# Kernel tuning notes

Measured on AMD Instinct MI355X. Metric: run time of the kernel, lower is better.

The kernel has to match this reference:

```python
import jax, jax.numpy as jnp
import numpy as np

N, E, B, L = 32768, 524288, 64, 512  # nodes, edges, graphs, max nodes/graph
V, D, H = 10000, 256, 512            # vocab, embed_dim, hidden_dim


def gcn_conv(h, W, b, src, dst, n):
    """PyG GCNConv: add self-loops, symmetric deg normalization, scatter-sum."""
    h = h @ W  # [n, out]
    loops = jnp.arange(n)
    s = jnp.concatenate([src, loops])
    d = jnp.concatenate([dst, loops])
    deg = jax.ops.segment_sum(jnp.ones_like(d, dtype=h.dtype), d, num_segments=n)
    dinv = jnp.where(deg > 0, jax.lax.rsqrt(deg), 0.0)
    norm = dinv[s] * dinv[d]  # [E+n]
    out = jax.ops.segment_sum(h[s] * norm[:, None], d, num_segments=n)
    return out + b


def gru_seq(x, Wih, Whh, bih, bhh):
    """torch nn.GRU (1 layer, batch_first). x: [B, T, H] -> outputs [T, B, H]."""
    def step(h, x_t):
        gi = x_t @ Wih.T + bih          # [B, 3H]
        gh = h @ Whh.T + bhh            # [B, 3H]
        ir, iz, inn = jnp.split(gi, 3, axis=-1)
        hr, hz, hn = jnp.split(gh, 3, axis=-1)
        r = jax.nn.sigmoid(ir + hr)
        z = jax.nn.sigmoid(iz + hz)
        n = jnp.tanh(inn + r * hn)
        h = (1.0 - z) * n + z * h
        return h, h
    h0 = jnp.zeros((x.shape[0], Whh.shape[1]), x.dtype)
    _, outs = jax.lax.scan(step, h0, jnp.swapaxes(x, 0, 1))
    return outs  # [T, B, H]


def setup_inputs() -> dict:
    key = jax.random.key(0)
    ks = jax.random.split(key, 16)
    s = 0.05
    x = jax.random.randint(ks[0], (N,), 0, V)
    edge_index = jax.random.randint(ks[1], (2, E), 0, N)
    batch_idx = jnp.arange(N) // L  # sorted graph ids, L nodes per graph
    focal_points = jax.random.uniform(ks[2], (B, 1), jnp.float32)
    return {
        "x": x, "edge_index": edge_index, "batch_idx": batch_idx,
        "focal_points": focal_points,
        "emb": jax.random.normal(ks[3], (V, D), jnp.float32) * s,
        "W1": jax.random.normal(ks[4], (D, H), jnp.float32) * s,
        "b1": jnp.zeros((H,), jnp.float32),
        "W2": jax.random.normal(ks[5], (H, H), jnp.float32) * s,
        "b2": jnp.zeros((H,), jnp.float32),
        "Wih": jax.random.normal(ks[6], (3 * H, H), jnp.float32) * s,
        "Whh": jax.random.normal(ks[7], (3 * H, H), jnp.float32) * s,
        "bih": jnp.zeros((3 * H,), jnp.float32),
        "bhh": jnp.zeros((3 * H,), jnp.float32),
        "fc1_w": jax.random.normal(ks[8], (H + 1, H), jnp.float32) * s,
        "fc1_b": jnp.zeros((H,), jnp.float32),
        "fc2_w": jax.random.normal(ks[9], (H, 1), jnp.float32) * s,
        "fc2_b": jnp.zeros((1,), jnp.float32),
    }


def reference(x, edge_index, batch_idx, focal_points, emb, W1, b1, W2, b2,
              Wih, Whh, bih, bhh, fc1_w, fc1_b, fc2_w, fc2_b):
    src, dst = edge_index[0], edge_index[1]
    h = emb[x]  # [N, D]
    h = jax.nn.relu(gcn_conv(h, W1, b1, src, dst, N))
    h = jax.nn.relu(gcn_conv(h, W2, b2, src, dst, N))  # [N, H]

    # Ragged -> padded: scatter each node to (graph, position-within-graph)
    ones = jnp.ones((N,), h.dtype)
    counts = jax.ops.segment_sum(ones, batch_idx, num_segments=B)
    starts = jnp.cumsum(counts) - counts  # exclusive cumsum
    pos = jnp.arange(N) - starts[batch_idx].astype(jnp.int32)
    padded = jnp.zeros((B, L, H), h.dtype).at[batch_idx, pos].set(h)

    gru_out = gru_seq(padded, Wih, Whh, bih, bhh)   # [L, B, H]
    graph_emb = gru_out.mean(axis=0)                # [B, H]
    g = jnp.concatenate([graph_emb, focal_points], axis=1)  # [B, H+1]
    out = jax.nn.relu(g @ fc1_w + fc1_b)
    out = jax.nn.sigmoid(out @ fc2_w + fc2_b)       # [B, 1]
    return out
```

## Files before the change

### kernel.cpp

```cpp
#include <hip/hip_runtime.h>

#define NODES 32768
#define EDGES 524288
#define BGR   64
#define LSEQ  512
#define DEMB  256
#define HDIM  512

typedef unsigned short u16;
typedef unsigned int   u32;
typedef unsigned long long u64;
typedef __attribute__((ext_vector_type(8))) short short8;
typedef __attribute__((ext_vector_type(4))) float f32x4;

__device__ __forceinline__ float bf2f(u16 u){ u32 x = ((u32)u)<<16; float f; __builtin_memcpy(&f,&x,4); return f; }
__device__ __forceinline__ u16 f2bf(float f){ u32 x; __builtin_memcpy(&x,&f,4); u32 r = x + 0x7fffu + ((x>>16)&1u); return (u16)(r>>16); }
__device__ __forceinline__ float lo16(u32 u){ u32 x = u<<16; float f; __builtin_memcpy(&f,&x,4); return f; }
__device__ __forceinline__ float hi16(u32 u){ u32 x = u & 0xffff0000u; float f; __builtin_memcpy(&f,&x,4); return f; }
__device__ __forceinline__ u32 pack2(float a, float b){ return (u32)f2bf(a) | ((u32)f2bf(b)<<16); }


__global__ void zero_i32(int* p, int n){
  int i = blockIdx.x*256 + threadIdx.x;
  if (i < n) p[i] = 0;
}

__global__ void transpose_cast(const float* __restrict__ in, u16* __restrict__ out, int K, int N){
  int i = blockIdx.x*256 + threadIdx.x;
  if (i < N*K){ int n = i / K, k = i - n*K; out[i] = f2bf(in[(size_t)k*N + n]); }
}

__global__ void cast_bf(const float* __restrict__ in, u16* __restrict__ out, int n){
  int i = blockIdx.x*256 + threadIdx.x;
  if (i < n) out[i] = f2bf(in[i]);
}

__global__ void count_indeg(const int* __restrict__ dst, int* __restrict__ indeg){
  int e = blockIdx.x*256 + threadIdx.x;
  if (e < EDGES) atomicAdd(&indeg[dst[e]], 1);
}

__global__ void compute_dinv(const int* __restrict__ indeg, float* __restrict__ dinv){
  int i = blockIdx.x*256 + threadIdx.x;
  if (i < NODES) dinv[i] = rsqrtf((float)(indeg[i] + 1));
}

__global__ __launch_bounds__(1024) void scan_csr(const int* __restrict__ indeg,
                                                 int* __restrict__ row_ptr,
                                                 int* __restrict__ cursor){
  __shared__ int part[1024];
  int tid = threadIdx.x, base = tid*32;
  int loc[32]; int s = 0;
  for (int i=0;i<32;i++){ loc[i] = s; s += indeg[base+i]; }
  part[tid] = s; __syncthreads();
  for (int off=1; off<1024; off<<=1){
    int v = part[tid]; int add = (tid>=off) ? part[tid-off] : 0;
    __syncthreads(); part[tid] = v + add; __syncthreads();
  }
  int offt = (tid==0) ? 0 : part[tid-1];
  for (int i=0;i<32;i++){ int v = offt + loc[i]; row_ptr[base+i] = v; cursor[base+i] = v; }
}

__global__ void fill_csr(const int* __restrict__ src, const int* __restrict__ dst,
                         int* __restrict__ cursor, int* __restrict__ csr_src){
  int e = blockIdx.x*256 + threadIdx.x;
  if (e < EDGES){ int d = dst[e]; int p = atomicAdd(&cursor[d], 1); csr_src[p] = src[e]; }
}

__global__ __launch_bounds__(256) void agg_emb(const int* __restrict__ x, const u16* __restrict__ embb,
    const float* __restrict__ dinv, const int* __restrict__ row_ptr, const int* __restrict__ indeg,
    const int* __restrict__ csr_src, u16* __restrict__ out){
  int node = blockIdx.x*4 + (threadIdx.x>>6);
  int lane = threadIdx.x & 63;
  float di = dinv[node];
  int xi = x[node];
  u64 hv = *(const u64*)(embb + (size_t)xi*DEMB + lane*4);
  u32 h0 = (u32)hv, h1 = (u32)(hv>>32);
  float a0 = lo16(h0)*di, a1 = hi16(h0)*di, a2 = lo16(h1)*di, a3 = hi16(h1)*di;
  int st = row_ptr[node], cn = indeg[node];
  for (int p = st; p < st+cn; p++){
    int s = csr_src[p];
    float ws = dinv[s];
    u64 v = *(const u64*)(embb + (size_t)x[s]*DEMB + lane*4);
    u32 w0 = (u32)v, w1 = (u32)(v>>32);
    a0 += lo16(w0)*ws; a1 += hi16(w0)*ws; a2 += lo16(w1)*ws; a3 += hi16(w1)*ws;
  }
  u64 pv = (u64)pack2(a0*di,a1*di) | ((u64)pack2(a2*di,a3*di)<<32);
  *(u64*)(out + (size_t)node*DEMB + lane*4) = pv;
}

__global__ __launch_bounds__(256) void agg_h(const u16* __restrict__ hin, const float* __restrict__ dinv,
    const int* __restrict__ row_ptr, const int* __restrict__ indeg,
    const int* __restrict__ csr_src, u16* __restrict__ out){
  int node = blockIdx.x*4 + (threadIdx.x>>6);
  int lane = threadIdx.x & 63;
  float di = dinv[node];
  float a[8];
  uint4 hv = *((const uint4*)(hin + (size_t)node*HDIM) + lane);
  a[0]=lo16(hv.x)*di; a[1]=hi16(hv.x)*di; a[2]=lo16(hv.y)*di; a[3]=hi16(hv.y)*di;
  a[4]=lo16(hv.z)*di; a[5]=hi16(hv.z)*di; a[6]=lo16(hv.w)*di; a[7]=hi16(hv.w)*di;
  int st = row_ptr[node], cn = indeg[node];
  for (int p = st; p < st+cn; p++){
    int s = csr_src[p];
    float ws = dinv[s];
    uint4 v = *((const uint4*)(hin + (size_t)s*HDIM) + lane);
    a[0]+=lo16(v.x)*ws; a[1]+=hi16(v.x)*ws; a[2]+=lo16(v.y)*ws; a[3]+=hi16(v.y)*ws;
    a[4]+=lo16(v.z)*ws; a[5]+=hi16(v.z)*ws; a[6]+=lo16(v.w)*ws; a[7]+=hi16(v.w)*ws;
  }
  uint4 o; o.x=pack2(a[0]*di,a[1]*di); o.y=pack2(a[2]*di,a[3]*di);
  o.z=pack2(a[4]*di,a[5]*di); o.w=pack2(a[6]*di,a[7]*di);
  *(uint4*)(out + (size_t)node*HDIM + lane*8) = o;
}

#define BM 128
#define BN 128
#define BKK 32
__global__ __launch_bounds__(256) void gemm_bt(const u16* __restrict__ A, const u16* __restrict__ BT,
    const float* __restrict__ bias, u16* __restrict__ C, int M, int N, int K, int relu){
  __shared__ u16 aS[BM][BKK+8];
  __shared__ u16 bS[BN][BKK+8];
  int tid = threadIdx.x;
  int m0 = blockIdx.y * BM, n0 = blockIdx.x * BN;
  int lane = tid & 63, w = tid >> 6;
  int wm = w >> 1, wn = w & 1;
  f32x4 acc[4][4];
  for (int i=0;i<4;i++) for (int j=0;j<4;j++) acc[i][j] = (f32x4)0.0f;

  int r  = tid >> 1;
  int cc = (tid & 1) * 16;
  const u16* Ag = A + (size_t)(m0 + r) * K + cc;
  const u16* Bg = BT + (size_t)(n0 + r) * K + cc;
  int l15 = lane & 15, q8 = (lane >> 4) * 8;

  for (int k0 = 0; k0 < K; k0 += BKK) {
    uint4 av0 = *(const uint4*)(Ag + k0);
    uint4 av1 = *(const uint4*)(Ag + k0 + 8);
    uint4 bv0 = *(const uint4*)(Bg + k0);
    uint4 bv1 = *(const uint4*)(Bg + k0 + 8);
    *(uint4*)&aS[r][cc]   = av0; *(uint4*)&aS[r][cc+8] = av1;
    *(uint4*)&bS[r][cc]   = bv0; *(uint4*)&bS[r][cc+8] = bv1;
    __syncthreads();
    short8 af[4], bfr[4];
    for (int i=0;i<4;i++) af[i]  = *(const short8*)&aS[wm*64 + i*16 + l15][q8];
    for (int j=0;j<4;j++) bfr[j] = *(const short8*)&bS[wn*64 + j*16 + l15][q8];
    for (int i=0;i<4;i++)
      for (int j=0;j<4;j++)
        acc[i][j] = __builtin_amdgcn_mfma_f32_16x16x32_bf16(af[i], bfr[j], acc[i][j], 0, 0, 0);
    __syncthreads();
  }
  int q = lane >> 4;
  for (int i=0;i<4;i++) for (int j=0;j<4;j++){
    int col = n0 + wn*64 + j*16 + l15;
    float bval = bias[col];
    for (int rr=0; rr<4; rr++){
      int row = m0 + wm*64 + i*16 + q*4 + rr;
      float v = acc[i][j][rr] + bval;
      if (relu) v = fmaxf(v, 0.f);
      C[(size_t)row * N + col] = f2bf(v);
    }
  }
}

__global__ __launch_bounds__(512) void gru_kernel(const u16* __restrict__ gi,
    const float* __restrict__ Whh, const float* __restrict__ bhh,
    float* __restrict__ graph_emb, u64* __restrict__ xbuf){
  __shared__ u16  w_lds[96*520];
  __shared__ u16  h_lds[16*520];
  __shared__ float gh_lds[16*100];

  int tid = threadIdx.x;
  int g = blockIdx.x >> 4, j = blockIdx.x & 15;
  int lane = tid & 63, wave = tid >> 6;

  for (int idx = tid; idx < 96*512; idx += 512){
    int rr = idx >> 9, c = idx & 511;
    int grow = (rr >> 5) * 512 + j*32 + (rr & 31);
    w_lds[rr*520 + c] = f2bf(Whh[(size_t)grow*512 + c]);
  }
  for (int idx = tid; idx < 16*520; idx += 512) h_lds[idx] = 0;

  int b = tid >> 5, hh = tid & 31;
  int bg = g*16 + b;
  int c_r = j*32 + hh, c_z = 512 + j*32 + hh, c_n = 1024 + j*32 + hh;
  float bias_r = bhh[c_r], bias_z = bhh[c_z], bias_n = bhh[c_n];
  const u16* gi_row = gi + (size_t)bg * LSEQ * 1536;
  float h_prev = 0.f, accm = 0.f;
  int l15 = lane & 15, q8 = (lane>>4)*8, qr = (lane>>4)*4;

  u64* xb = xbuf + (size_t)g * 8192;
  u16 g_r = gi_row[c_r], g_z = gi_row[c_z], g_n = gi_row[c_n];

  __syncthreads();

  for (int t = 0; t < LSEQ; t++){
    if (wave < 6){
      f32x4 acc0 = (f32x4)0.0f, acc1 = (f32x4)0.0f;
      const u16* wrow = &w_lds[(wave*16 + l15)*520];
      const u16* hrow = &h_lds[l15*520];
      #pragma unroll
      for (int k0 = 0; k0 < 256; k0 += 32){
        acc0 = __builtin_amdgcn_mfma_f32_16x16x32_bf16(*(const short8*)(hrow + k0 + q8),
                                                       *(const short8*)(wrow + k0 + q8), acc0, 0, 0, 0);
        acc1 = __builtin_amdgcn_mfma_f32_16x16x32_bf16(*(const short8*)(hrow + 256 + k0 + q8),
                                                       *(const short8*)(wrow + 256 + k0 + q8), acc1, 0, 0, 0);
      }
      f32x4 acc = acc0 + acc1;
      int col = wave*16 + l15;
      #pragma unroll
      for (int rr2 = 0; rr2 < 4; rr2++) gh_lds[(qr + rr2)*100 + col] = acc[rr2];
    }
    __syncthreads();

    float ghr = gh_lds[b*100 + hh]      + bias_r;
    float ghz = gh_lds[b*100 + 32 + hh] + bias_z;
    float ghn = gh_lds[b*100 + 64 + hh] + bias_n;
    float rg = 1.f / (1.f + __expf(-(bf2f(g_r) + ghr)));
    float zg = 1.f / (1.f + __expf(-(bf2f(g_z) + ghz)));
    float pre = bf2f(g_n) + rg * ghn;
    pre = fminf(fmaxf(pre, -20.f), 20.f);
    float e2 = __expf(2.f * pre);
    float nn = (e2 - 1.f) / (e2 + 1.f);
    float h_new = (1.f - zg) * nn + zg * h_prev;
    accm += h_new; h_prev = h_new;

    u32 tag = (u32)(t + 1);
    float h_nb = __shfl_xor(h_new, 1, 64);
    if ((hh & 1) == 0){
      u64 val = ((u64)tag << 32) | (u64)pack2(h_new, h_nb);
      __hip_atomic_store(xb + (size_t)((t&1)*16 + b)*256 + j*16 + (hh>>1), val,
                         __ATOMIC_RELAXED, __HIP_MEMORY_SCOPE_AGENT);
    }

    int tn = (t + 1 < LSEQ) ? t + 1 : t;
    const u16* gp2 = gi_row + (size_t)tn * 1536;
    u16 n_r = gp2[c_r], n_z = gp2[c_z], n_n = gp2[c_n];

    const u64* rp = xb + (size_t)((t&1)*16 + b)*256 + hh*8;
    u64 v[8];
    bool ok;
    do {
      #pragma unroll
      for (int i=0;i<8;i++) v[i] = __hip_atomic_load(rp + i, __ATOMIC_RELAXED, __HIP_MEMORY_SCOPE_AGENT);
      ok = true;
      #pragma unroll
      for (int i=0;i<8;i++) ok = ok && ((u32)(v[i] >> 32) == tag);
    } while (!ok);

    u32* hl = (u32*)h_lds + b*260 + hh*8;
    #pragma unroll
    for (int i=0;i<8;i++) hl[i] = (u32)v[i];
    __syncthreads();

    g_r = n_r; g_z = n_z; g_n = n_n;
  }
  graph_emb[(size_t)bg*512 + j*32 + hh] = accm * (1.f/512.f);
}

__global__ __launch_bounds__(256) void head(const float* __restrict__ graph_emb, const float* __restrict__ focal,
    const float* __restrict__ fc1w, const float* __restrict__ fc1b,
    const float* __restrict__ fc2w, const float* __restrict__ fc2b, float* __restrict__ out){
  __shared__ float gv[513];
  __shared__ float h1s[512];
  __shared__ float red[4];
  int bq = blockIdx.x, tid = threadIdx.x;
  for (int i = tid; i < 512; i += 256) gv[i] = graph_emb[(size_t)bq*512 + i];
  if (tid == 0) gv[512] = focal[bq];
  __syncthreads();
  for (int c = tid; c < 512; c += 256){
    float acc = fc1b[c];
    for (int k = 0; k < 513; k++) acc += gv[k] * fc1w[(size_t)k*512 + c];
    h1s[c] = fmaxf(acc, 0.f);
  }
  __syncthreads();
  float p = h1s[tid]*fc2w[tid] + h1s[tid+256]*fc2w[tid+256];
  for (int off = 32; off; off >>= 1) p += __shfl_down(p, off, 64);
  if ((tid & 63) == 0) red[tid >> 6] = p;
  __syncthreads();
  if (tid == 0){
    float s = red[0]+red[1]+red[2]+red[3] + fc2b[0];
    out[bq] = 1.f / (1.f + __expf(-s));
  }
}

extern "C" void kernel_launch(void* const* d_in, const int* in_sizes, int n_in,
                              void* d_out, int out_size, void* d_ws, size_t ws_size,
                              hipStream_t stream){
  const int*   x     = (const int*)d_in[0];
  const int*   edge  = (const int*)d_in[1];
  const int*   srcp  = edge;
  const int*   dstp  = edge + EDGES;
  const float* focal = (const float*)d_in[3];
  const float* emb   = (const float*)d_in[4];
  const float* W1    = (const float*)d_in[5];
  const float* b1    = (const float*)d_in[6];
  const float* W2    = (const float*)d_in[7];
  const float* b2    = (const float*)d_in[8];
  const float* Wih   = (const float*)d_in[9];
  const float* Whh   = (const float*)d_in[10];
  const float* bih   = (const float*)d_in[11];
  const float* bhh   = (const float*)d_in[12];
  const float* fc1w  = (const float*)d_in[13];
  const float* fc1b  = (const float*)d_in[14];
  const float* fc2w  = (const float*)d_in[15];
  const float* fc2b  = (const float*)d_in[16];

  char* ws = (char*)d_ws;
  constexpr size_t H2_OFF    = 0;
  constexpr size_t AGG1_OFF  = 33554432;
  constexpr size_t H1_OFF    = 50331648;
  constexpr size_t AGG2_OFF  = 83886080;
  constexpr size_t GI_OFF    = 33554432;
  constexpr size_t MISC      = 134217728;
  constexpr size_t INDEG_OFF = MISC;
  constexpr size_t CNT_OFF   = MISC + 131072;
  constexpr size_t DINV_OFF  = MISC + 131328;
  constexpr size_t ROWPTR_OFF= MISC + 262400;
  constexpr size_t CURSOR_OFF= MISC + 393472;
  constexpr size_t CSR_OFF   = MISC + 524544;
  constexpr size_t W1T_OFF   = MISC + 2621696;
  constexpr size_t W2T_OFF   = MISC + 2883840;
  constexpr size_t WIHB_OFF  = MISC + 3408128;
  constexpr size_t XBUF_OFF  = MISC + 4980992;
  constexpr size_t GEMB_OFF  = MISC + 5243136;

  int*   indeg  = (int*)(ws + INDEG_OFF);
  float* dinv   = (float*)(ws + DINV_OFF);
  int*   rowptr = (int*)(ws + ROWPTR_OFF);
  int*   cursor = (int*)(ws + CURSOR_OFF);
  int*   csrsrc = (int*)(ws + CSR_OFF);
  u16*   W1T    = (u16*)(ws + W1T_OFF);
  u16*   W2T    = (u16*)(ws + W2T_OFF);
  u16*   WihB   = (u16*)(ws + WIHB_OFF);
  u16*   agg1   = (u16*)(ws + AGG1_OFF);
  u16*   h1     = (u16*)(ws + H1_OFF);
  u16*   agg2   = (u16*)(ws + AGG2_OFF);
  u16*   embb   = (u16*)(ws + AGG2_OFF);
  u16*   h2     = (u16*)(ws + H2_OFF);
  u16*   gi     = (u16*)(ws + GI_OFF);
  u64*   xbuf   = (u64*)(ws + XBUF_OFF);
  float* gemb   = (float*)(ws + GEMB_OFF);

  zero_i32<<<129, 256, 0, stream>>>(indeg, 32768 + 64);
  transpose_cast<<<512, 256, 0, stream>>>(W1, W1T, 256, 512);
  transpose_cast<<<1024, 256, 0, stream>>>(W2, W2T, 512, 512);
  cast_bf<<<3072, 256, 0, stream>>>(Wih, WihB, 1536*512);
  cast_bf<<<10000, 256, 0, stream>>>(emb, embb, 10000*256);
  count_indeg<<<2048, 256, 0, stream>>>(dstp, indeg);
  compute_dinv<<<128, 256, 0, stream>>>(indeg, dinv);
  scan_csr<<<1, 1024, 0, stream>>>(indeg, rowptr, cursor);
  fill_csr<<<2048, 256, 0, stream>>>(srcp, dstp, cursor, csrsrc);
  agg_emb<<<8192, 256, 0, stream>>>(x, embb, dinv, rowptr, indeg, csrsrc, agg1);
  gemm_bt<<<dim3(4, 256), 256, 0, stream>>>(agg1, W1T, b1, h1, NODES, 512, 256, 1);
  agg_h<<<8192, 256, 0, stream>>>(h1, dinv, rowptr, indeg, csrsrc, agg2);
  gemm_bt<<<dim3(4, 256), 256, 0, stream>>>(agg2, W2T, b2, h2, NODES, 512, 512, 1);
  gemm_bt<<<dim3(12, 256), 256, 0, stream>>>(h2, WihB, bih, gi, NODES, 1536, 512, 0);
  gru_kernel<<<64, 512, 0, stream>>>(gi, Whh, bhh, gemb, xbuf);
  head<<<64, 256, 0, stream>>>(gemb, focal, fc1w, fc1b, fc2w, fc2b, (float*)d_out);
}
```

Before: 2.587 ms.

## Pre-swizzle GRU weights and hidden state in LDS, double-buffer h, prefetch gi two steps ahead

Stores the recurrent weight slice and the hidden state in LDS in an MFMA-fragment-major layout, padded to 65 entries, so each lane does one contiguous 16-byte load per operand with fewer bank conflicts. The hidden state is double-buffered by timestep parity, and each lane writes its received values as two uint4 stores. The input-gate values are now prefetched two steps ahead instead of one to hide global load latency in the serial recurrence. An unused offset constant is removed. The cost is extra registers and a more complex indexing scheme.

```diff
diff --git a/kernel.cpp b/kernel.cpp
--- a/kernel.cpp
+++ b/kernel.cpp
@@ -164,20 +164,26 @@
 __global__ __launch_bounds__(512) void gru_kernel(const u16* __restrict__ gi,
     const float* __restrict__ Whh, const float* __restrict__ bhh,
     float* __restrict__ graph_emb, u64* __restrict__ xbuf){
-  __shared__ u16  w_lds[96*520];
-  __shared__ u16  h_lds[16*520];
+  __shared__ __align__(16) u16 w_swz[6*16*65*8];
+  __shared__ __align__(16) u16 h_swz[2][16*65*8];
   __shared__ float gh_lds[16*100];
 
   int tid = threadIdx.x;
   int g = blockIdx.x >> 4, j = blockIdx.x & 15;
   int lane = tid & 63, wave = tid >> 6;
-
-  for (int idx = tid; idx < 96*512; idx += 512){
-    int rr = idx >> 9, c = idx & 511;
-    int grow = (rr >> 5) * 512 + j*32 + (rr & 31);
-    w_lds[rr*520 + c] = f2bf(Whh[(size_t)grow*512 + c]);
-  }
-  for (int idx = tid; idx < 16*520; idx += 512) h_lds[idx] = 0;
+  int l15 = lane & 15, qr = (lane>>4)*4;
+
+  for (int s = tid; s < 6144; s += 512){
+    int w = s >> 10, rem = s & 1023, kc = rem >> 6, l = rem & 63;
+    int row = l & 15, qq = l >> 4;
+    int gate = w >> 1, half = w & 1;
+    int c = gate*512 + j*32 + half*16 + row;
+    const float* srcp = Whh + (size_t)c*512 + kc*32 + qq*8;
+    u16* dst = w_swz + ((size_t)(w*16 + kc)*65 + l)*8;
+    #pragma unroll
+    for (int i2 = 0; i2 < 8; i2++) dst[i2] = f2bf(srcp[i2]);
+  }
+  for (int i2 = tid; i2 < 16*65*8; i2 += 512) h_swz[0][i2] = 0;
 
   int b = tid >> 5, hh = tid & 31;
   int bg = g*16 + b;
@@ -185,24 +191,36 @@
   float bias_r = bhh[c_r], bias_z = bhh[c_z], bias_n = bhh[c_n];
   const u16* gi_row = gi + (size_t)bg * LSEQ * 1536;
   float h_prev = 0.f, accm = 0.f;
-  int l15 = lane & 15, q8 = (lane>>4)*8, qr = (lane>>4)*4;
 
   u64* xb = xbuf + (size_t)g * 8192;
-  u16 g_r = gi_row[c_r], g_z = gi_row[c_z], g_n = gi_row[c_n];
+
+  u16 gr0 = gi_row[c_r], gz0 = gi_row[c_z], gn0 = gi_row[c_n];
+  const u16* gp1 = gi_row + 1536;
+  u16 gr1 = gp1[c_r], gz1 = gp1[c_z], gn1 = gp1[c_n];
+
+  int kcc = hh >> 1, qa = (hh & 1) * 2;
+  int cb0 = (kcc*65 + (qa  )*16 + b) * 4;
+  int cb1 = (kcc*65 + (qa+1)*16 + b) * 4;
 
   __syncthreads();
 
   for (int t = 0; t < LSEQ; t++){
+    int tn = (t + 2 < LSEQ) ? t + 2 : t;
+    const u16* gp2 = gi_row + (size_t)tn * 1536;
+    u16 nr = gp2[c_r], nz = gp2[c_z], nn2 = gp2[c_n];
+
     if (wave < 6){
+      const u16* hb = h_swz[t & 1];
+      const u16* wb = w_swz + (size_t)wave*16*65*8;
       f32x4 acc0 = (f32x4)0.0f, acc1 = (f32x4)0.0f;
-      const u16* wrow = &w_lds[(wave*16 + l15)*520];
-      const u16* hrow = &h_lds[l15*520];
       #pragma unroll
-      for (int k0 = 0; k0 < 256; k0 += 32){
-        acc0 = __builtin_amdgcn_mfma_f32_16x16x32_bf16(*(const short8*)(hrow + k0 + q8),
-                                                       *(const short8*)(wrow + k0 + q8), acc0, 0, 0, 0);
-        acc1 = __builtin_amdgcn_mfma_f32_16x16x32_bf16(*(const short8*)(hrow + 256 + k0 + q8),
-                                                       *(const short8*)(wrow + 256 + k0 + q8), acc1, 0, 0, 0);
+      for (int kc = 0; kc < 8; kc++){
+        acc0 = __builtin_amdgcn_mfma_f32_16x16x32_bf16(
+                 *(const short8*)(hb + ((size_t)kc*65 + lane)*8),
+                 *(const short8*)(wb + ((size_t)kc*65 + lane)*8), acc0, 0, 0, 0);
+        acc1 = __builtin_amdgcn_mfma_f32_16x16x32_bf16(
+                 *(const short8*)(hb + ((size_t)(kc+8)*65 + lane)*8),
+                 *(const short8*)(wb + ((size_t)(kc+8)*65 + lane)*8), acc1, 0, 0, 0);
       }
       f32x4 acc = acc0 + acc1;
       int col = wave*16 + l15;
@@ -214,9 +232,9 @@
     float ghr = gh_lds[b*100 + hh]      + bias_r;
     float ghz = gh_lds[b*100 + 32 + hh] + bias_z;
     float ghn = gh_lds[b*100 + 64 + hh] + bias_n;
-    float rg = 1.f / (1.f + __expf(-(bf2f(g_r) + ghr)));
-    float zg = 1.f / (1.f + __expf(-(bf2f(g_z) + ghz)));
-    float pre = bf2f(g_n) + rg * ghn;
+    float rg = 1.f / (1.f + __expf(-(bf2f(gr0) + ghr)));
+    float zg = 1.f / (1.f + __expf(-(bf2f(gz0) + ghz)));
+    float pre = bf2f(gn0) + rg * ghn;
     pre = fminf(fmaxf(pre, -20.f), 20.f);
     float e2 = __expf(2.f * pre);
     float nn = (e2 - 1.f) / (e2 + 1.f);
@@ -230,10 +248,6 @@
       __hip_atomic_store(xb + (size_t)((t&1)*16 + b)*256 + j*16 + (hh>>1), val,
                          __ATOMIC_RELAXED, __HIP_MEMORY_SCOPE_AGENT);
     }
-
-    int tn = (t + 1 < LSEQ) ? t + 1 : t;
-    const u16* gp2 = gi_row + (size_t)tn * 1536;
-    u16 n_r = gp2[c_r], n_z = gp2[c_z], n_n = gp2[c_n];
 
     const u64* rp = xb + (size_t)((t&1)*16 + b)*256 + hh*8;
     u64 v[8];
@@ -246,12 +260,15 @@
       for (int i=0;i<8;i++) ok = ok && ((u32)(v[i] >> 32) == tag);
     } while (!ok);
 
-    u32* hl = (u32*)h_lds + b*260 + hh*8;
-    #pragma unroll
-    for (int i=0;i<8;i++) hl[i] = (u32)v[i];
+    u32* hl = (u32*)h_swz[(t+1) & 1];
+    uint4 w0; w0.x = (u32)v[0]; w0.y = (u32)v[1]; w0.z = (u32)v[2]; w0.w = (u32)v[3];
+    uint4 w1; w1.x = (u32)v[4]; w1.y = (u32)v[5]; w1.z = (u32)v[6]; w1.w = (u32)v[7];
+    *(uint4*)(hl + cb0) = w0;
+    *(uint4*)(hl + cb1) = w1;
     __syncthreads();
 
-    g_r = n_r; g_z = n_z; g_n = n_n;
+    gr0 = gr1; gz0 = gz1; gn0 = gn1;
+    gr1 = nr;  gz1 = nz;  gn1 = nn2;
   }
   graph_emb[(size_t)bg*512 + j*32 + hh] = accm * (1.f/512.f);
 }
@@ -312,7 +329,6 @@
   constexpr size_t GI_OFF    = 33554432;
   constexpr size_t MISC      = 134217728;
   constexpr size_t INDEG_OFF = MISC;
-  constexpr size_t CNT_OFF   = MISC + 131072;
   constexpr size_t DINV_OFF  = MISC + 131328;
   constexpr size_t ROWPTR_OFF= MISC + 262400;
   constexpr size_t CURSOR_OFF= MISC + 393472;
```

After: 2.729 ms. 1.05x slower.

## Split GRU recurrence across twice as many blocks with K-split MFMA waves

Applied to the files above, without the earlier changes.

The persistent GRU kernel now uses 32 blocks per group of 16 graphs instead of 16, so each block owns 16 hidden columns rather than 32. The six waves now split the K dimension in half per gate, writing two partial gh buffers that are summed in the gate computation. This shortens each block's per-step serial matvec chain and spreads the work over more CUs. In exchange, the cross-block flag exchange each step involves more participants, and half the threads sit idle during the gate math. It also vectorizes the LDS writes of the exchanged hidden state.

```diff
diff --git a/kernel.cpp b/kernel.cpp
--- a/kernel.cpp
+++ b/kernel.cpp
@@ -164,78 +164,84 @@
 __global__ __launch_bounds__(512) void gru_kernel(const u16* __restrict__ gi,
     const float* __restrict__ Whh, const float* __restrict__ bhh,
     float* __restrict__ graph_emb, u64* __restrict__ xbuf){
-  __shared__ u16  w_lds[96*520];
+  __shared__ u16  w_lds[48*520];
   __shared__ u16  h_lds[16*520];
-  __shared__ float gh_lds[16*100];
+  __shared__ float gh_lds[2][16*52];
 
   int tid = threadIdx.x;
-  int g = blockIdx.x >> 4, j = blockIdx.x & 15;
+  int g = blockIdx.x >> 5, j = blockIdx.x & 31;
   int lane = tid & 63, wave = tid >> 6;
-
-  for (int idx = tid; idx < 96*512; idx += 512){
+  int l15 = lane & 15, q8 = (lane>>4)*8, qr = (lane>>4)*4;
+
+  for (int idx = tid; idx < 48*512; idx += 512){
     int rr = idx >> 9, c = idx & 511;
-    int grow = (rr >> 5) * 512 + j*32 + (rr & 31);
+    int grow = (rr >> 4) * 512 + j*16 + (rr & 15);
     w_lds[rr*520 + c] = f2bf(Whh[(size_t)grow*512 + c]);
   }
   for (int idx = tid; idx < 16*520; idx += 512) h_lds[idx] = 0;
 
-  int b = tid >> 5, hh = tid & 31;
-  int bg = g*16 + b;
-  int c_r = j*32 + hh, c_z = 512 + j*32 + hh, c_n = 1024 + j*32 + hh;
-  float bias_r = bhh[c_r], bias_z = bhh[c_z], bias_n = bhh[c_n];
+  int b = tid >> 4, hh = tid & 15;
+  int bg = g*16 + (b & 15);
+  int c_r = j*16 + hh, c_z = 512 + j*16 + hh, c_n = 1024 + j*16 + hh;
+  float bias_r = 0.f, bias_z = 0.f, bias_n = 0.f;
+  if (tid < 256){ bias_r = bhh[c_r]; bias_z = bhh[c_z]; bias_n = bhh[c_n]; }
   const u16* gi_row = gi + (size_t)bg * LSEQ * 1536;
   float h_prev = 0.f, accm = 0.f;
-  int l15 = lane & 15, q8 = (lane>>4)*8, qr = (lane>>4)*4;
+
+  int pb = tid >> 5, ph = tid & 31;
 
   u64* xb = xbuf + (size_t)g * 8192;
-  u16 g_r = gi_row[c_r], g_z = gi_row[c_z], g_n = gi_row[c_n];
+
+  u16 gr0 = 0, gz0 = 0, gn0 = 0;
+  if (tid < 256){ gr0 = gi_row[c_r]; gz0 = gi_row[c_z]; gn0 = gi_row[c_n]; }
 
   __syncthreads();
 
   for (int t = 0; t < LSEQ; t++){
     if (wave < 6){
-      f32x4 acc0 = (f32x4)0.0f, acc1 = (f32x4)0.0f;
-      const u16* wrow = &w_lds[(wave*16 + l15)*520];
-      const u16* hrow = &h_lds[l15*520];
+      int gate = wave >> 1, kh = wave & 1;
+      const u16* wrow = &w_lds[(gate*16 + l15)*520 + kh*256];
+      const u16* hrow = &h_lds[l15*520 + kh*256];
+      f32x4 acc = (f32x4)0.0f;
       #pragma unroll
-      for (int k0 = 0; k0 < 256; k0 += 32){
-        acc0 = __builtin_amdgcn_mfma_f32_16x16x32_bf16(*(const short8*)(hrow + k0 + q8),
-                                                       *(const short8*)(wrow + k0 + q8), acc0, 0, 0, 0);
-        acc1 = __builtin_amdgcn_mfma_f32_16x16x32_bf16(*(const short8*)(hrow + 256 + k0 + q8),
-                                                       *(const short8*)(wrow + 256 + k0 + q8), acc1, 0, 0, 0);
-      }
-      f32x4 acc = acc0 + acc1;
-      int col = wave*16 + l15;
+      for (int kc = 0; kc < 8; kc++)
+        acc = __builtin_amdgcn_mfma_f32_16x16x32_bf16(*(const short8*)(hrow + kc*32 + q8),
+                                                      *(const short8*)(wrow + kc*32 + q8), acc, 0, 0, 0);
+      int col = gate*16 + l15;
       #pragma unroll
-      for (int rr2 = 0; rr2 < 4; rr2++) gh_lds[(qr + rr2)*100 + col] = acc[rr2];
+      for (int rr2 = 0; rr2 < 4; rr2++) gh_lds[kh][(qr + rr2)*52 + col] = acc[rr2];
     }
     __syncthreads();
 
-    float ghr = gh_lds[b*100 + hh]      + bias_r;
-    float ghz = gh_lds[b*100 + 32 + hh] + bias_z;
-    float ghn = gh_lds[b*100 + 64 + hh] + bias_n;
-    float rg = 1.f / (1.f + __expf(-(bf2f(g_r) + ghr)));
-    float zg = 1.f / (1.f + __expf(-(bf2f(g_z) + ghz)));
-    float pre = bf2f(g_n) + rg * ghn;
-    pre = fminf(fmaxf(pre, -20.f), 20.f);
-    float e2 = __expf(2.f * pre);
-    float nn = (e2 - 1.f) / (e2 + 1.f);
-    float h_new = (1.f - zg) * nn + zg * h_prev;
-    accm += h_new; h_prev = h_new;
-
     u32 tag = (u32)(t + 1);
-    float h_nb = __shfl_xor(h_new, 1, 64);
-    if ((hh & 1) == 0){
-      u64 val = ((u64)tag << 32) | (u64)pack2(h_new, h_nb);
-      __hip_atomic_store(xb + (size_t)((t&1)*16 + b)*256 + j*16 + (hh>>1), val,
-                         __ATOMIC_RELAXED, __HIP_MEMORY_SCOPE_AGENT);
+    int par = t & 1;
+
+    if (tid < 256){
+      float ghr = gh_lds[0][b*52 + hh]      + gh_lds[1][b*52 + hh]      + bias_r;
+      float ghz = gh_lds[0][b*52 + 16 + hh] + gh_lds[1][b*52 + 16 + hh] + bias_z;
+      float ghn = gh_lds[0][b*52 + 32 + hh] + gh_lds[1][b*52 + 32 + hh] + bias_n;
+      float rg = 1.f / (1.f + __expf(-(bf2f(gr0) + ghr)));
+      float zg = 1.f / (1.f + __expf(-(bf2f(gz0) + ghz)));
+      float pre = bf2f(gn0) + rg * ghn;
+      pre = fminf(fmaxf(pre, -20.f), 20.f);
+      float e2 = __expf(2.f * pre);
+      float nn = (e2 - 1.f) / (e2 + 1.f);
+      float h_new = (1.f - zg) * nn + zg * h_prev;
+      accm += h_new; h_prev = h_new;
+
+      float h_nb = __shfl_xor(h_new, 1, 64);
+      if ((hh & 1) == 0){
+        u64 val = ((u64)tag << 32) | (u64)pack2(h_new, h_nb);
+        __hip_atomic_store(xb + (size_t)(par*16 + b)*256 + j*8 + (hh>>1), val,
+                           __ATOMIC_RELAXED, __HIP_MEMORY_SCOPE_AGENT);
+      }
+
+      int tn = (t + 1 < LSEQ) ? t + 1 : t;
+      const u16* gp2 = gi_row + (size_t)tn * 1536;
+      gr0 = gp2[c_r]; gz0 = gp2[c_z]; gn0 = gp2[c_n];
     }
 
-    int tn = (t + 1 < LSEQ) ? t + 1 : t;
-    const u16* gp2 = gi_row + (size_t)tn * 1536;
-    u16 n_r = gp2[c_r], n_z = gp2[c_z], n_n = gp2[c_n];
-
-    const u64* rp = xb + (size_t)((t&1)*16 + b)*256 + hh*8;
+    const u64* rp = xb + (size_t)(par*16 + pb)*256 + ph*8;
     u64 v[8];
     bool ok;
     do {
@@ -246,14 +252,15 @@
       for (int i=0;i<8;i++) ok = ok && ((u32)(v[i] >> 32) == tag);
     } while (!ok);
 
-    u32* hl = (u32*)h_lds + b*260 + hh*8;
-    #pragma unroll
-    for (int i=0;i<8;i++) hl[i] = (u32)v[i];
+    u32* hl = (u32*)h_lds + pb*260 + ph*8;
+    uint4 w0; w0.x=(u32)v[0]; w0.y=(u32)v[1]; w0.z=(u32)v[2]; w0.w=(u32)v[3];
+    uint4 w1; w1.x=(u32)v[4]; w1.y=(u32)v[5]; w1.z=(u32)v[6]; w1.w=(u32)v[7];
+    *(uint4*)hl = w0;
+    *((uint4*)hl + 1) = w1;
     __syncthreads();
-
-    g_r = n_r; g_z = n_z; g_n = n_n;
-  }
-  graph_emb[(size_t)bg*512 + j*32 + hh] = accm * (1.f/512.f);
+  }
+  if (tid < 256)
+    graph_emb[(size_t)bg*512 + j*16 + hh] = accm * (1.f/512.f);
 }
 
 __global__ __launch_bounds__(256) void head(const float* __restrict__ graph_emb, const float* __restrict__ focal,
@@ -312,7 +319,6 @@
   constexpr size_t GI_OFF    = 33554432;
   constexpr size_t MISC      = 134217728;
   constexpr size_t INDEG_OFF = MISC;
-  constexpr size_t CNT_OFF   = MISC + 131072;
   constexpr size_t DINV_OFF  = MISC + 131328;
   constexpr size_t ROWPTR_OFF= MISC + 262400;
   constexpr size_t CURSOR_OFF= MISC + 393472;
@@ -354,6 +360,6 @@
   agg_h<<<8192, 256, 0, stream>>>(h1, dinv, rowptr, indeg, csrsrc, agg2);
   gemm_bt<<<dim3(4, 256), 256, 0, stream>>>(agg2, W2T, b2, h2, NODES, 512, 512, 1);
   gemm_bt<<<dim3(12, 256), 256, 0, stream>>>(h2, WihB, bih, gi, NODES, 1536, 512, 0);
-  gru_kernel<<<64, 512, 0, stream>>>(gi, Whh, bhh, gemb, xbuf);
+  gru_kernel<<<128, 512, 0, stream>>>(gi, Whh, bhh, gemb, xbuf);
   head<<<64, 256, 0, stream>>>(gemb, focal, fc1w, fc1b, fc2w, fc2b, (float*)d_out);
 }
```

After: 2.983 ms. 1.15x slower.
